# Kernel tuning notes

Measured on AMD Instinct MI355X. Metric: run time of the kernel, lower is better.

Reference implementation:

```python
import jax, jax.numpy as jnp
import numpy as np

N_OUT = 100000 - 1  # 99999, as hard-coded in the torch module
LEAK = 0.01         # torch LeakyReLU default slope


def setup_inputs() -> dict:
    key = jax.random.key(0)
    k1, k2, k3, k4, k5 = jax.random.split(key, 5)
    B, D = 512, 512
    H = D // 2
    x = jax.random.normal(k1, (B, D), dtype=jnp.float32)
    # torch.nn.Linear-style init scale ~ 1/sqrt(fan_in)
    w2 = jax.random.normal(k2, (H, D), dtype=jnp.float32) / np.sqrt(D)
    b2 = jax.random.normal(k3, (H,), dtype=jnp.float32) / np.sqrt(D)
    w3 = jax.random.normal(k4, (55, H), dtype=jnp.float32) / np.sqrt(H)
    b3 = jax.random.normal(k5, (55,), dtype=jnp.float32) / np.sqrt(H)
    return {"x": x, "w2": w2, "b2": b2, "w3": w3, "b3": b3}


def _digit_tables():
    # Static integer tables for i in [0, N_OUT).
    i = np.arange(N_OUT, dtype=np.int32)
    ndig = ((i >= 10).astype(np.int32) + (i >= 100) + (i >= 1000) + (i >= 10000)).astype(np.int32)
    ndig[0] = 1  # special case in the original code: i==0 -> n=1
    return jnp.asarray(i), jnp.asarray(ndig)


def reference(x, w2, b2, w3, b3):
    # tiny MLP (batched; equivalent to the per-sample torch loop)
    h = x @ w2.T + b2
    h = jnp.where(h >= 0, h, LEAK * h)          # LeakyReLU
    z = h @ w3.T + b3                            # [B, 55]
    p_len = jax.nn.softmax(z[:, :5], axis=-1)    # length distribution (5)
    p_dig = jax.nn.softmax(z[:, 5:].reshape(-1, 5, 10), axis=-1)  # 5 digit groups of 10
    x3 = jnp.concatenate([p_len, p_dig.reshape(-1, 50)], axis=-1)  # [B, 55]

    i, ndig = _digit_tables()                    # [N], [N]
    out = jnp.take(x3, ndig, axis=1)             # lead factor x3[k, n_i] -> [B, N]
    # Multiply the first n_i digit probabilities (original drops the last digit).
    for j in range(4):                           # max usable digits: n<=4
        expo = jnp.maximum(ndig - j, 0)
        d = (i // jnp.power(10, expo)) % 10      # j-th most significant digit
        idx = 5 + d + 10 * j                     # index into x3 digit groups
        factor = jnp.take(x3, idx, axis=1)       # [B, N]
        valid = (j < ndig)[None, :]
        out = out * jnp.where(valid, factor, 1.0)
    return out
```

## Files before the change

kernel.cpp:

```cpp
#include <hip/hip_runtime.h>
#include <hip/hip_bf16.h>


#define BATCH 512
#define DIM   512
#define HID   256
#define NCLS  55
#define NOUT  99999
#define LEAK  0.01f

__device__ __forceinline__ float digit_factor(
    unsigned i, const float* __restrict__ T4A, const float* __restrict__ T3A,
    const float* __restrict__ T2A, const float* __restrict__ B4,
    const float* __restrict__ B3, const float* __restrict__ A1x, float row0) {
    if (i >= 10000u) {
        unsigned t = i / 10u;
        unsigned q = t / 100u;
        unsigned r = t - q * 100u;
        return T4A[q] * B4[r];
    } else if (i >= 1000u) {
        unsigned t = i / 10u;
        unsigned q = t / 10u;
        unsigned d = t - q * 10u;
        return T3A[q] * B3[d];
    } else if (i >= 100u) {
        return T2A[i / 10u];
    } else if (i >= 10u || i == 0u) {
        return A1x[i / 10u];
    }
    return row0;
}

__global__ __launch_bounds__(256) void fused_mlp_expand(
    const float* __restrict__ x,  const float* __restrict__ w2,
    const float* __restrict__ b2, const float* __restrict__ w3,
    const float* __restrict__ b3, float* __restrict__ out) {
    __shared__ float xs[DIM];
    __shared__ float hs[HID];
    __shared__ float zp[4][NCLS];
    __shared__ float x3s[NCLS];
    __shared__ float T4A[100], T3A[100], T2A[100], B4[100];
    __shared__ float B3[10], A1x[10];

    const int tid = threadIdx.x;
    const int k   = blockIdx.x;

    xs[tid]       = x[(size_t)k * DIM + tid];
    xs[tid + 256] = x[(size_t)k * DIM + tid + 256];
    __syncthreads();

    {
        const float4* w2r = (const float4*)(w2 + (size_t)tid * DIM);
        const float4* xr  = (const float4*)xs;
        float acc = 0.f;
#pragma unroll 8
        for (int d4 = 0; d4 < DIM / 4; ++d4) {
            float4 w  = w2r[d4];
            float4 xv = xr[d4];
            acc += w.x * xv.x + w.y * xv.y + w.z * xv.z + w.w * xv.w;
        }
        acc += b2[tid];
        hs[tid] = (acc >= 0.f) ? acc : LEAK * acc;
    }
    __syncthreads();

    if (tid < 4 * NCLS) {
        int o = tid % NCLS, part = tid / NCLS;
        const float4* w3r = (const float4*)(w3 + (size_t)o * HID + part * 64);
        const float4* hr  = (const float4*)(hs + part * 64);
        float a = 0.f;
#pragma unroll
        for (int d4 = 0; d4 < 16; ++d4) {
            float4 w = w3r[d4];
            float4 h = hr[d4];
            a += w.x * h.x + w.y * h.y + w.z * h.z + w.w * h.w;
        }
        zp[part][o] = a;
    }
    __syncthreads();
    if (tid < NCLS)
        x3s[tid] = zp[0][tid] + zp[1][tid] + zp[2][tid] + zp[3][tid] + b3[tid];
    __syncthreads();

    if (tid < 6) {
        int off = (tid == 0) ? 0 : 5 + 10 * (tid - 1);
        int len = (tid == 0) ? 5 : 10;
        float m = -1e30f;
        for (int u = 0; u < len; ++u) m = fmaxf(m, x3s[off + u]);
        float s = 0.f;
        for (int u = 0; u < len; ++u) {
            float e = __expf(x3s[off + u] - m);
            x3s[off + u] = e;
            s += e;
        }
        float inv = 1.f / s;
        for (int u = 0; u < len; ++u) x3s[off + u] *= inv;
    }
    __syncthreads();

    for (int q = tid; q < 100; q += 256) {
        int hi = q / 10, lo = q % 10;
        float pp = x3s[5 + hi] * x3s[15 + lo];
        T4A[q] = x3s[4] * pp;
        T3A[q] = x3s[3] * pp;
        T2A[q] = x3s[2] * pp;
        B4[q]  = x3s[25 + hi] * x3s[35 + lo];
    }
    if (tid < 10) {
        B3[tid]  = x3s[25 + tid];
        A1x[tid] = x3s[1] * x3s[5 + tid];
    }
    __syncthreads();

    const float row0 = x3s[0];

    const size_t base = (size_t)k * NOUT;
    const unsigned head = (unsigned)((4 - (base & 3)) & 3);
    const unsigned ng = (NOUT - head) >> 2;
    const unsigned tail_start = head + (ng << 2);

    if (tid < (int)head)
        out[base + tid] = digit_factor((unsigned)tid, T4A, T3A, T2A, B4, B3, A1x, row0);
    if (tid < (int)(NOUT - tail_start)) {
        unsigned i = tail_start + (unsigned)tid;
        out[base + i] = digit_factor(i, T4A, T3A, T2A, B4, B3, A1x, row0);
    }

    float4* outv = (float4*)(out + base + head);
    for (unsigned g = tid; g < ng; g += 256) {
        unsigned i0 = head + (g << 2);
        float4 v;
        v.x = digit_factor(i0,      T4A, T3A, T2A, B4, B3, A1x, row0);
        v.y = digit_factor(i0 + 1u, T4A, T3A, T2A, B4, B3, A1x, row0);
        v.z = digit_factor(i0 + 2u, T4A, T3A, T2A, B4, B3, A1x, row0);
        v.w = digit_factor(i0 + 3u, T4A, T3A, T2A, B4, B3, A1x, row0);
        outv[g] = v;
    }
}

extern "C" void kernel_launch(void* const* d_in, const int* in_sizes, int n_in,
                              void* d_out, int out_size, void* d_ws, size_t ws_size,
                              hipStream_t stream) {
    const float* x  = (const float*)d_in[0];
    const float* w2 = (const float*)d_in[1];
    const float* b2 = (const float*)d_in[2];
    const float* w3 = (const float*)d_in[3];
    const float* b3 = (const float*)d_in[4];
    float* out = (float*)d_out;

    fused_mlp_expand<<<BATCH, 256, 0, stream>>>(x, w2, b2, w3, b3, out);
}
```

Baseline: 244.0 us.

## Split MLP and expansion into two kernels with 8x more expansion blocks

New measurement: 244.6 us. No clear change (+0.2%).

```diff
diff --git a/kernel.cpp b/kernel.cpp
--- a/kernel.cpp
+++ b/kernel.cpp
@@ -9,38 +9,14 @@
 #define NOUT  99999
 #define LEAK  0.01f
 
-__device__ __forceinline__ float digit_factor(
-    unsigned i, const float* __restrict__ T4A, const float* __restrict__ T3A,
-    const float* __restrict__ T2A, const float* __restrict__ B4,
-    const float* __restrict__ B3, const float* __restrict__ A1x, float row0) {
-    if (i >= 10000u) {
-        unsigned t = i / 10u;
-        unsigned q = t / 100u;
-        unsigned r = t - q * 100u;
-        return T4A[q] * B4[r];
-    } else if (i >= 1000u) {
-        unsigned t = i / 10u;
-        unsigned q = t / 10u;
-        unsigned d = t - q * 10u;
-        return T3A[q] * B3[d];
-    } else if (i >= 100u) {
-        return T2A[i / 10u];
-    } else if (i >= 10u || i == 0u) {
-        return A1x[i / 10u];
-    }
-    return row0;
-}
-
-__global__ __launch_bounds__(256) void fused_mlp_expand(
+__global__ __launch_bounds__(256) void mlp_x3_kernel(
     const float* __restrict__ x,  const float* __restrict__ w2,
     const float* __restrict__ b2, const float* __restrict__ w3,
-    const float* __restrict__ b3, float* __restrict__ out) {
+    const float* __restrict__ b3, float* __restrict__ x3out) {
     __shared__ float xs[DIM];
     __shared__ float hs[HID];
     __shared__ float zp[4][NCLS];
     __shared__ float x3s[NCLS];
-    __shared__ float T4A[100], T3A[100], T2A[100], B4[100];
-    __shared__ float B3[10], A1x[10];
 
     const int tid = threadIdx.x;
     const int k   = blockIdx.x;
@@ -52,14 +28,15 @@
     {
         const float4* w2r = (const float4*)(w2 + (size_t)tid * DIM);
         const float4* xr  = (const float4*)xs;
-        float acc = 0.f;
+        float4 a4 = make_float4(0.f, 0.f, 0.f, 0.f);
 #pragma unroll 8
         for (int d4 = 0; d4 < DIM / 4; ++d4) {
             float4 w  = w2r[d4];
             float4 xv = xr[d4];
-            acc += w.x * xv.x + w.y * xv.y + w.z * xv.z + w.w * xv.w;
+            a4.x += w.x * xv.x; a4.y += w.y * xv.y;
+            a4.z += w.z * xv.z; a4.w += w.w * xv.w;
         }
-        acc += b2[tid];
+        float acc = (a4.x + a4.y) + (a4.z + a4.w) + b2[tid];
         hs[tid] = (acc >= 0.f) ? acc : LEAK * acc;
     }
     __syncthreads();
@@ -68,14 +45,15 @@
         int o = tid % NCLS, part = tid / NCLS;
         const float4* w3r = (const float4*)(w3 + (size_t)o * HID + part * 64);
         const float4* hr  = (const float4*)(hs + part * 64);
-        float a = 0.f;
+        float4 a4 = make_float4(0.f, 0.f, 0.f, 0.f);
 #pragma unroll
         for (int d4 = 0; d4 < 16; ++d4) {
             float4 w = w3r[d4];
             float4 h = hr[d4];
-            a += w.x * h.x + w.y * h.y + w.z * h.z + w.w * h.w;
+            a4.x += w.x * h.x; a4.y += w.y * h.y;
+            a4.z += w.z * h.z; a4.w += w.w * h.w;
         }
-        zp[part][o] = a;
+        zp[part][o] = (a4.x + a4.y) + (a4.z + a4.w);
     }
     __syncthreads();
     if (tid < NCLS)
@@ -98,42 +76,81 @@
     }
     __syncthreads();
 
-    for (int q = tid; q < 100; q += 256) {
-        int hi = q / 10, lo = q % 10;
+    if (tid < NCLS) x3out[k * NCLS + tid] = x3s[tid];
+}
+
+__device__ __forceinline__ float Vj(
+    unsigned j, const float* __restrict__ T4A, const float* __restrict__ T3A,
+    const float* __restrict__ T2A, const float* __restrict__ B4,
+    const float* __restrict__ B3,  const float* __restrict__ A1b) {
+    if (j >= 1000u) { unsigned q = j / 100u; return T4A[q] * B4[j - q * 100u]; }
+    if (j >= 100u)  { unsigned q = j / 10u;  return T3A[q] * B3[j - q * 10u]; }
+    if (j >= 10u)   return T2A[j];
+    return A1b[j];
+}
+
+__global__ __launch_bounds__(256) void expand_kernel(
+    const float* __restrict__ x3g, float* __restrict__ out) {
+    __shared__ float T4A[100], T3A[100], T2A[100], B4[100];
+    __shared__ float B3[16], A1b[16];
+    __shared__ float x3s[NCLS];
+
+    const int tid = threadIdx.x;
+    const int k   = blockIdx.x >> 3;
+    const int s   = blockIdx.x & 7;
+
+    if (tid < NCLS) x3s[tid] = x3g[k * NCLS + tid];
+    __syncthreads();
+
+    if (tid < 100) {
+        int hi = tid / 10, lo = tid % 10;
         float pp = x3s[5 + hi] * x3s[15 + lo];
-        T4A[q] = x3s[4] * pp;
-        T3A[q] = x3s[3] * pp;
-        T2A[q] = x3s[2] * pp;
-        B4[q]  = x3s[25 + hi] * x3s[35 + lo];
-    }
-    if (tid < 10) {
-        B3[tid]  = x3s[25 + tid];
-        A1x[tid] = x3s[1] * x3s[5 + tid];
+        T4A[tid] = x3s[4] * pp;
+        T3A[tid] = x3s[3] * pp;
+        T2A[tid] = x3s[2] * pp;
+        B4[tid]  = x3s[25 + hi] * x3s[35 + lo];
+    } else if (tid < 110) {
+        int d = tid - 100;
+        B3[d]  = x3s[25 + d];
+        A1b[d] = (d == 0) ? x3s[0] : x3s[1] * x3s[5 + d];
     }
     __syncthreads();
 
-    const float row0 = x3s[0];
+    const float pz = x3s[1] * x3s[5];
 
-    const size_t base = (size_t)k * NOUT;
-    const unsigned head = (unsigned)((4 - (base & 3)) & 3);
-    const unsigned ng = (NOUT - head) >> 2;
-    const unsigned tail_start = head + (ng << 2);
+    const unsigned e_lo = (unsigned)s * 12500u;
+    const unsigned n_el = (s == 7) ? 12499u : 12500u;
+    const size_t   gbase = (size_t)k * NOUT + e_lo;
+    const unsigned head = (unsigned)((4u - ((unsigned)gbase & 3u)) & 3u);
+    const unsigned ng   = (n_el - head) >> 2;
+    const unsigned tail0 = head + (ng << 2);
 
-    if (tid < (int)head)
-        out[base + tid] = digit_factor((unsigned)tid, T4A, T3A, T2A, B4, B3, A1x, row0);
-    if (tid < (int)(NOUT - tail_start)) {
-        unsigned i = tail_start + (unsigned)tid;
-        out[base + i] = digit_factor(i, T4A, T3A, T2A, B4, B3, A1x, row0);
+    if (tid < (int)head) {
+        unsigned i = e_lo + (unsigned)tid;
+        float v = Vj(i / 10u, T4A, T3A, T2A, B4, B3, A1b);
+        if (i == 0u) v = pz;
+        out[gbase + tid] = v;
+    }
+    if (tid < (int)(n_el - tail0)) {
+        unsigned e = tail0 + (unsigned)tid;
+        unsigned i = e_lo + e;
+        out[gbase + e] = Vj(i / 10u, T4A, T3A, T2A, B4, B3, A1b);
     }
 
-    float4* outv = (float4*)(out + base + head);
+    float4* outv = (float4*)(out + gbase + head);
     for (unsigned g = tid; g < ng; g += 256) {
-        unsigned i0 = head + (g << 2);
+        unsigned i   = e_lo + head + (g << 2);
+        unsigned j0  = i / 10u;
+        unsigned rem = i - j0 * 10u;
+        float v0 = Vj(j0, T4A, T3A, T2A, B4, B3, A1b);
+        unsigned j1 = j0 + (rem >= 7u ? 1u : 0u);
+        float v1 = Vj(j1, T4A, T3A, T2A, B4, B3, A1b);
+        unsigned m = 10u - rem;
         float4 v;
-        v.x = digit_factor(i0,      T4A, T3A, T2A, B4, B3, A1x, row0);
-        v.y = digit_factor(i0 + 1u, T4A, T3A, T2A, B4, B3, A1x, row0);
-        v.z = digit_factor(i0 + 2u, T4A, T3A, T2A, B4, B3, A1x, row0);
-        v.w = digit_factor(i0 + 3u, T4A, T3A, T2A, B4, B3, A1x, row0);
+        v.x = (i == 0u) ? pz : v0;
+        v.y = (1u < m) ? v0 : v1;
+        v.z = (2u < m) ? v0 : v1;
+        v.w = (3u < m) ? v0 : v1;
         outv[g] = v;
     }
 }
@@ -147,6 +164,8 @@
     const float* w3 = (const float*)d_in[3];
     const float* b3 = (const float*)d_in[4];
     float* out = (float*)d_out;
+    float* x3  = (float*)d_ws;
 
-    fused_mlp_expand<<<BATCH, 256, 0, stream>>>(x, w2, b2, w3, b3, out);
+    mlp_x3_kernel<<<BATCH, 256, 0, stream>>>(x, w2, b2, w3, b3, x3);
+    expand_kernel<<<BATCH * 8, 256, 0, stream>>>(x3, out);
 }
```
